# Kernel tuning notes

Measured on AMD Instinct MI355X. Metric: run time of the kernel, lower is better.

## Reference

```python
import jax, jax.numpy as jnp
import numpy as np

B, N, C, H = 4, 2048, 1024, 16
HD = C // H            # head dim = 64
HALF = HD // 2         # complex pairs per head = 32
VR = 32.0              # virtual_resolution
THETA = 10.0           # rope_theta


def _init_freqs():
    # mirrors init_3d_freqs_unified + per-axis replication with small noise
    rng = np.random.default_rng(0)
    idx = np.arange(HALF, dtype=np.float32)
    base = 1.0 / THETA ** (2.0 * idx / HD)                 # [HALF]
    angles = rng.uniform(0, 2 * np.pi, size=(H, 1)).astype(np.float32)
    per_head = base[None, :] * np.cos(angles)              # [H, HALF]
    freqs = np.repeat(per_head[None], 3, axis=0)           # [3, H, HALF]
    freqs = freqs + rng.normal(0, 0.01, freqs.shape).astype(np.float32)
    return jnp.asarray(freqs.reshape(3, H * HALF), dtype=jnp.float32)


def setup_inputs() -> dict:
    key = jax.random.key(0)
    ks = jax.random.split(key, 7)
    x = jax.random.normal(ks[0], (B, N, C), dtype=jnp.float32)
    t_x = jax.random.uniform(ks[1], (N,), dtype=jnp.float32)
    t_y = jax.random.uniform(ks[2], (N,), dtype=jnp.float32)
    t_z = jax.random.uniform(ks[3], (N,), dtype=jnp.float32)
    w_qkv = jax.random.normal(ks[4], (3 * C, C), dtype=jnp.float32) * (C ** -0.5)
    w_proj = jax.random.normal(ks[5], (C, C), dtype=jnp.float32) * (C ** -0.5)
    b_proj = jnp.zeros((C,), dtype=jnp.float32)
    freqs = _init_freqs()
    return {"x": x, "t_x": t_x, "t_y": t_y, "t_z": t_z,
            "w_qkv": w_qkv, "w_proj": w_proj, "b_proj": b_proj, "freqs": freqs}


def _normalize(t):
    # normalize_point_coords_3d with 'virtual_resolution'
    return (t - t.min()) / (t.max() - t.min() + 1e-8) * VR


def reference(x, t_x, t_y, t_z, w_qkv, w_proj, b_proj, freqs):
    # QKV projection (no bias)
    qkv = (x @ w_qkv.T).reshape(B, N, 3, H, HD).transpose(2, 0, 3, 1, 4)  # [3,B,H,N,HD]
    q, k, v = qkv[0], qkv[1], qkv[2]

    # mixed 3D RoPE angles: outer(t_axis, freqs[axis]) summed over axes
    tx, ty, tz = _normalize(t_x), _normalize(t_y), _normalize(t_z)
    ang = (tx[:, None] * freqs[0] + ty[:, None] * freqs[1] + tz[:, None] * freqs[2])  # [N, H*HALF]
    ang = ang.reshape(N, H, HALF).transpose(1, 0, 2)       # [H, N, HALF]
    cos, sin = jnp.cos(ang), jnp.sin(ang)

    def rotate(t):
        # complex multiply (a+ib)*(cos+isin) on even/odd pairs of last dim
        tr = t.reshape(B, H, N, HALF, 2)
        a, b = tr[..., 0], tr[..., 1]
        ra = a * cos - b * sin
        rb = a * sin + b * cos
        return jnp.stack([ra, rb], axis=-1).reshape(B, H, N, HD)

    q = rotate(q)
    k = rotate(k)

    scale = HD ** -0.5
    attn = jax.nn.softmax(jnp.einsum('bhnd,bhmd->bhnm', q * scale, k), axis=-1)
    out = jnp.einsum('bhnm,bhmd->bhnd', attn, v).transpose(0, 2, 1, 3).reshape(B, N, C)
    return out @ w_proj.T + b_proj
```

## Files before the change

kernel.cpp:

```cpp
#include <hip/hip_runtime.h>
#include <math.h>

#define BB 4
#define NN 2048
#define CC 1024
#define HH 16
#define HD 64
#define HALF 32
#define MM (BB*NN)
#define K3 (3*CC)
#define NF (HH*HALF)
#define NT (NN/64)

typedef __attribute__((ext_vector_type(8))) short bf16x8;
typedef __attribute__((ext_vector_type(4))) float f32x4;
typedef __attribute__((ext_vector_type(16))) float f32x16;
typedef __attribute__((ext_vector_type(4))) unsigned short u16x4;
typedef __attribute__((ext_vector_type(8))) unsigned short u16x8;
typedef __attribute__((ext_vector_type(4))) unsigned int u32x4;

#if __has_builtin(__builtin_amdgcn_exp2f)
#define EXP2(x) __builtin_amdgcn_exp2f(x)
#else
#define EXP2(x) exp2f(x)
#endif
#define AS1 __attribute__((address_space(1)))
#define AS3 __attribute__((address_space(3)))

__device__ __forceinline__ unsigned short f2bf(float f) {
    unsigned int u = __float_as_uint(f);
    unsigned int r = (u + 0x7FFFu + ((u >> 16) & 1u)) >> 16;
    return (unsigned short)r;
}

__global__ __launch_bounds__(256) void tnorm_kernel(const float* t_x, const float* t_y,
                                                    const float* t_z, float* tnorm) {
    int a = blockIdx.x;
    const float* t = (a == 0) ? t_x : ((a == 1) ? t_y : t_z);
    __shared__ float smn[256], smx[256];
    float mn = 1e30f, mx = -1e30f;
    for (int i = threadIdx.x; i < NN; i += 256) {
        float v = t[i];
        mn = fminf(mn, v);
        mx = fmaxf(mx, v);
    }
    smn[threadIdx.x] = mn; smx[threadIdx.x] = mx;
    __syncthreads();
    for (int s = 128; s > 0; s >>= 1) {
        if (threadIdx.x < s) {
            smn[threadIdx.x] = fminf(smn[threadIdx.x], smn[threadIdx.x + s]);
            smx[threadIdx.x] = fmaxf(smx[threadIdx.x], smx[threadIdx.x + s]);
        }
        __syncthreads();
    }
    float lo = smn[0];
    float sc = 32.0f / (smx[0] - lo + 1e-8f);
    for (int i = threadIdx.x; i < NN; i += 256)
        tnorm[a * NN + i] = (t[i] - lo) * sc;
}

__global__ __launch_bounds__(512) void angle_kernel(const float* freqs, const float* tnorm,
                                                    float* csT) {
    int n = blockIdx.x;
    int hf = threadIdx.x;
    float ang = tnorm[n] * freqs[hf]
              + tnorm[NN + n] * freqs[NF + hf]
              + tnorm[2 * NN + n] * freqs[2 * NF + hf];
    float2 cs;
    cs.x = cosf(ang);
    cs.y = sinf(ang);
    *(float2*)(csT + 2 * ((size_t)n * NF + hf)) = cs;
}

__global__ __launch_bounds__(256) void cvt_kernel(const float* __restrict__ src,
                                                  unsigned short* __restrict__ dst, int n) {
    int i = (blockIdx.x * 256 + threadIdx.x) * 8;
    if (i < n) {
        float4 a = *(const float4*)(src + i);
        float4 b = *(const float4*)(src + i + 4);
        u16x8 o;
        o[0] = f2bf(a.x); o[1] = f2bf(a.y); o[2] = f2bf(a.z); o[3] = f2bf(a.w);
        o[4] = f2bf(b.x); o[5] = f2bf(b.y); o[6] = f2bf(b.z); o[7] = f2bf(b.w);
        *(u16x8*)(dst + i) = o;
    }
}

__global__ __launch_bounds__(256) void qkv_gemm_kernel(const unsigned short* __restrict__ A,
                                                       const unsigned short* __restrict__ Bw,
                                                       const float* __restrict__ csT,
                                                       unsigned short* __restrict__ qb,
                                                       unsigned short* __restrict__ kb,
                                                       unsigned short* __restrict__ vbT) {
    __shared__ unsigned short Asl[128 * 64];
    __shared__ unsigned short Bsl[128 * 64];
    const int tid = threadIdx.x;
    const int wv = tid >> 6, l = tid & 63;
    const int wm = wv >> 1, wn = wv & 1;
    const int lg = l >> 4, l15 = l & 15;
    const int bid = blockIdx.x;
    const int wgid = (bid & 7) * 192 + (bid >> 3);
    const int m0 = (wgid & 63) * 128;
    const int n0 = (wgid >> 6) * 128;

    f32x4 acc[4][4];
#pragma unroll
    for (int i = 0; i < 4; i++)
#pragma unroll
        for (int j = 0; j < 4; j++) acc[i][j] = f32x4{0.f, 0.f, 0.f, 0.f};

    for (int kt = 0; kt < CC; kt += 64) {
        __syncthreads();
#pragma unroll
        for (int i = 0; i < 4; i++) {
            int c = (wv * 4 + i) * 64 + l;
            int r = c >> 3, kc = c & 7;
            int sc = kt + ((kc ^ (r & 7)) * 8);
            __builtin_amdgcn_global_load_lds(
                (AS1 void*)(A + (size_t)(m0 + r) * CC + sc),
                (AS3 void*)(&Asl[(wv * 4 + i) * 512]), 16, 0, 0);
            __builtin_amdgcn_global_load_lds(
                (AS1 void*)(Bw + (size_t)(n0 + r) * CC + sc),
                (AS3 void*)(&Bsl[(wv * 4 + i) * 512]), 16, 0, 0);
        }
        __syncthreads();
#pragma unroll
        for (int kc = 0; kc < 2; kc++) {
            bf16x8 af[4], bfr[4];
#pragma unroll
            for (int mi = 0; mi < 4; mi++) {
                int r = wm * 64 + mi * 16 + l15;
                af[mi] = *(const bf16x8*)(&Asl[r * 64 + (((kc * 4 + lg) ^ (r & 7)) * 8)]);
            }
#pragma unroll
            for (int nj = 0; nj < 4; nj++) {
                int r = wn * 64 + nj * 16 + l15;
                bfr[nj] = *(const bf16x8*)(&Bsl[r * 64 + (((kc * 4 + lg) ^ (r & 7)) * 8)]);
            }
#pragma unroll
            for (int mi = 0; mi < 4; mi++)
#pragma unroll
                for (int nj = 0; nj < 4; nj++)
                    acc[mi][nj] = __builtin_amdgcn_mfma_f32_16x16x32_bf16(af[mi], bfr[nj], acc[mi][nj], 0, 0, 0);
        }
    }
    const int b_ = m0 >> 11;
    const int nrow0 = (m0 & (NN - 1));
#pragma unroll
    for (int nj = 0; nj < 4; nj++) {
        int oc = n0 + wn * 64 + nj * 16 + l15;
        int s = oc >> 10;
        int rr = oc & 1023;
        int h = rr >> 6;
        int d = rr & 63;
        int f = d >> 1;
#pragma unroll
        for (int mi = 0; mi < 4; mi++) {
            f32x4 v = acc[mi][nj];
            if (s == 2) {
                u16x4 vv;
#pragma unroll
                for (int reg = 0; reg < 4; reg++) vv[reg] = f2bf(v[reg]);
                int nb = nrow0 + wm * 64 + mi * 16 + lg * 4;
                *(u16x4*)(vbT + ((size_t)((b_ * HH + h) * HD + d)) * NN + nb) = vv;
            } else {
#pragma unroll
                for (int reg = 0; reg < 4; reg++) {
                    int m = m0 + wm * 64 + mi * 16 + lg * 4 + reg;
                    int n = m & (NN - 1);
                    float val = v[reg];
                    float partner = __shfl_xor(val, 1);
                    size_t base = (((size_t)(b_ * HH + h)) * NN + n) * HD + d;
                    float2 cs2 = *(const float2*)(csT + 2 * ((size_t)n * NF + h * HALF + f));
                    float res = ((d & 1) == 0) ? (val * cs2.x - partner * cs2.y)
                                               : (val * cs2.x + partner * cs2.y);
                    if (s == 0) res *= 0.18033688011112043f;
                    (s == 0 ? qb : kb)[base] = f2bf(res);
                }
            }
        }
    }
}

template<int BUF>
__device__ __forceinline__ void attn_iter(
    unsigned short* LB, bool do_stage, int wv, int l31,
    const unsigned short*& kn0, const unsigned short*& kn1,
    const unsigned short*& vn0, const unsigned short*& vn1,
    const int (&so)[4], const bf16x8 (&qfA)[4], const bf16x8 (&qfB)[4],
    const f32x16& Z, const bf16x8& ones,
    f32x16& OA0, f32x16& OA1, f32x16& OB0, f32x16& OB1,
    f32x16& SsA, f32x16& SsB) {
    if (do_stage) {
        const int nb = (BUF ^ 1) * 4096;
        __builtin_amdgcn_global_load_lds((AS1 void*)kn0, (AS3 void*)(&LB[nb + (wv * 2 + 0) * 512]), 16, 0, 0);
        __builtin_amdgcn_global_load_lds((AS1 void*)kn1, (AS3 void*)(&LB[nb + (wv * 2 + 1) * 512]), 16, 0, 0);
        __builtin_amdgcn_global_load_lds((AS1 void*)vn0, (AS3 void*)(&LB[8192 + nb + (wv * 2 + 0) * 512]), 16, 0, 0);
        __builtin_amdgcn_global_load_lds((AS1 void*)vn1, (AS3 void*)(&LB[8192 + nb + (wv * 2 + 1) * 512]), 16, 0, 0);
        kn0 += 4096; kn1 += 4096; vn0 += 64; vn1 += 64;
    }
    f32x16 sA0, sA1, sB0, sB1;
    __builtin_amdgcn_s_setprio(1);
    {
        bf16x8 a0 = *(const bf16x8*)(LB + BUF * 4096 + l31 * 64 + so[0]);
        bf16x8 a1 = *(const bf16x8*)(LB + BUF * 4096 + (32 + l31) * 64 + so[0]);
        sA0 = __builtin_amdgcn_mfma_f32_32x32x16_bf16(a0, qfA[0], Z, 0, 0, 0);
        sA1 = __builtin_amdgcn_mfma_f32_32x32x16_bf16(a1, qfA[0], Z, 0, 0, 0);
        sB0 = __builtin_amdgcn_mfma_f32_32x32x16_bf16(a0, qfB[0], Z, 0, 0, 0);
        sB1 = __builtin_amdgcn_mfma_f32_32x32x16_bf16(a1, qfB[0], Z, 0, 0, 0);
    }
#pragma unroll
    for (int dc = 1; dc < 4; dc++) {
        bf16x8 a0 = *(const bf16x8*)(LB + BUF * 4096 + l31 * 64 + so[dc]);
        bf16x8 a1 = *(const bf16x8*)(LB + BUF * 4096 + (32 + l31) * 64 + so[dc]);
        sA0 = __builtin_amdgcn_mfma_f32_32x32x16_bf16(a0, qfA[dc], sA0, 0, 0, 0);
        sA1 = __builtin_amdgcn_mfma_f32_32x32x16_bf16(a1, qfA[dc], sA1, 0, 0, 0);
        sB0 = __builtin_amdgcn_mfma_f32_32x32x16_bf16(a0, qfB[dc], sB0, 0, 0, 0);
        sB1 = __builtin_amdgcn_mfma_f32_32x32x16_bf16(a1, qfB[dc], sB1, 0, 0, 0);
    }
    __builtin_amdgcn_s_setprio(0);
#pragma unroll
    for (int r = 0; r < 16; r++) {
        sA0[r] = EXP2(sA0[r]); sA1[r] = EXP2(sA1[r]);
        sB0[r] = EXP2(sB0[r]); sB1[r] = EXP2(sB1[r]);
    }
#pragma unroll
    for (int r = 0; r < 8; r++) {
        unsigned u0, u1, u2, u3;
        asm("v_cvt_pk_bf16_f32 %0, %1, %2" : "=v"(u0) : "v"(sA0[2 * r]), "v"(sA0[2 * r + 1]));
        asm("v_cvt_pk_bf16_f32 %0, %1, %2" : "=v"(u1) : "v"(sA1[2 * r]), "v"(sA1[2 * r + 1]));
        asm("v_cvt_pk_bf16_f32 %0, %1, %2" : "=v"(u2) : "v"(sB0[2 * r]), "v"(sB0[2 * r + 1]));
        asm("v_cvt_pk_bf16_f32 %0, %1, %2" : "=v"(u3) : "v"(sB1[2 * r]), "v"(sB1[2 * r + 1]));
        sA0[2 * r] = __uint_as_float(u0);
        sA1[2 * r] = __uint_as_float(u1);
        sB0[2 * r] = __uint_as_float(u2);
        sB1[2 * r] = __uint_as_float(u3);
    }
    __builtin_amdgcn_s_setprio(1);
#pragma unroll
    for (int kc = 0; kc < 4; kc++) {
        const int bs = (kc & 1) * 8;
        bf16x8 pfA, pfB;
        {
            float e0 = (kc < 2) ? sA0[bs + 0] : sA1[bs + 0];
            float e4 = (kc < 2) ? sA0[bs + 4] : sA1[bs + 4];
            float e2 = (kc < 2) ? sA0[bs + 2] : sA1[bs + 2];
            float e6 = (kc < 2) ? sA0[bs + 6] : sA1[bs + 6];
            auto uA = __builtin_amdgcn_permlane32_swap(__float_as_uint(e0), __float_as_uint(e4), false, false);
            auto uB = __builtin_amdgcn_permlane32_swap(__float_as_uint(e2), __float_as_uint(e6), false, false);
            u32x4 t; t.x = uA[0]; t.y = uB[0]; t.z = uA[1]; t.w = uB[1];
            pfA = __builtin_bit_cast(bf16x8, t);
        }
        {
            float e0 = (kc < 2) ? sB0[bs + 0] : sB1[bs + 0];
            float e4 = (kc < 2) ? sB0[bs + 4] : sB1[bs + 4];
            float e2 = (kc < 2) ? sB0[bs + 2] : sB1[bs + 2];
            float e6 = (kc < 2) ? sB0[bs + 6] : sB1[bs + 6];
            auto uA = __builtin_amdgcn_permlane32_swap(__float_as_uint(e0), __float_as_uint(e4), false, false);
            auto uB = __builtin_amdgcn_permlane32_swap(__float_as_uint(e2), __float_as_uint(e6), false, false);
            u32x4 t; t.x = uA[0]; t.y = uB[0]; t.z = uA[1]; t.w = uB[1];
            pfB = __builtin_bit_cast(bf16x8, t);
        }
        bf16x8 va  = *(const bf16x8*)(LB + 8192 + BUF * 4096 + l31 * 64 + so[kc]);
        bf16x8 vb2 = *(const bf16x8*)(LB + 8192 + BUF * 4096 + (32 + l31) * 64 + so[kc]);
        OA0 = __builtin_amdgcn_mfma_f32_32x32x16_bf16(va,  pfA, OA0, 0, 0, 0);
        OA1 = __builtin_amdgcn_mfma_f32_32x32x16_bf16(vb2, pfA, OA1, 0, 0, 0);
        OB0 = __builtin_amdgcn_mfma_f32_32x32x16_bf16(va,  pfB, OB0, 0, 0, 0);
        OB1 = __builtin_amdgcn_mfma_f32_32x32x16_bf16(vb2, pfB, OB1, 0, 0, 0);
        SsA = __builtin_amdgcn_mfma_f32_32x32x16_bf16(ones, pfA, SsA, 0, 0, 0);
        SsB = __builtin_amdgcn_mfma_f32_32x32x16_bf16(ones, pfB, SsB, 0, 0, 0);
    }
    __builtin_amdgcn_s_setprio(0);
    __syncthreads();
}

__global__ __launch_bounds__(256, 2) void attn_mfma_kernel(const unsigned short* __restrict__ qbp,
                                                           const unsigned short* __restrict__ kbp,
                                                           const unsigned short* __restrict__ vtp,
                                                           unsigned short* __restrict__ aout) {
    __shared__ unsigned short LB[4 * 4096];
    const int tid = threadIdx.x;
    const int wv = tid >> 6;
    const int l = tid & 63;
    const int l31 = l & 31, hi = l >> 5;

    const int wg = blockIdx.x;
    const int Lidx = (wg & 7) * 64 + (wg >> 3);
    const int bh = Lidx >> 3;
    const int q0 = (Lidx & 7) * 256;

    const unsigned short* qp = qbp + (size_t)bh * (NN * HD);
    const unsigned short* kp = kbp + (size_t)bh * (NN * HD);
    const unsigned short* vp = vtp + (size_t)bh * (NN * HD);

    const int r0 = (wv * 2 + 0) * 8 + (l >> 3);
    const int r1 = (wv * 2 + 1) * 8 + (l >> 3);
    const int c0 = ((l & 7) ^ (r0 & 7)) * 8;
    const int c1 = ((l & 7) ^ (r1 & 7)) * 8;
    const unsigned short* kn0 = kp + r0 * HD + c0;
    const unsigned short* kn1 = kp + r1 * HD + c1;
    const unsigned short* vn0 = vp + (size_t)r0 * NN + c0;
    const unsigned short* vn1 = vp + (size_t)r1 * NN + c1;

    __builtin_amdgcn_global_load_lds((AS1 void*)kn0, (AS3 void*)(&LB[(wv * 2 + 0) * 512]), 16, 0, 0);
    __builtin_amdgcn_global_load_lds((AS1 void*)kn1, (AS3 void*)(&LB[(wv * 2 + 1) * 512]), 16, 0, 0);
    __builtin_amdgcn_global_load_lds((AS1 void*)vn0, (AS3 void*)(&LB[8192 + (wv * 2 + 0) * 512]), 16, 0, 0);
    __builtin_amdgcn_global_load_lds((AS1 void*)vn1, (AS3 void*)(&LB[8192 + (wv * 2 + 1) * 512]), 16, 0, 0);
    kn0 += 4096; kn1 += 4096; vn0 += 64; vn1 += 64;

    const unsigned short* qr = qp + (size_t)(q0 + wv * 64 + l31) * HD;
    bf16x8 qfA[4], qfB[4];
#pragma unroll
    for (int dc = 0; dc < 4; dc++) {
        qfA[dc] = *(const bf16x8*)(qr + dc * 16 + hi * 8);
        qfB[dc] = *(const bf16x8*)(qr + 32 * HD + dc * 16 + hi * 8);
    }

    int so[4];
#pragma unroll
    for (int i = 0; i < 4; i++) so[i] = ((2 * i + hi) ^ (l31 & 7)) * 8;

    f32x16 Z;
#pragma unroll
    for (int r = 0; r < 16; r++) Z[r] = 0.0f;
    f32x16 OA0 = Z, OA1 = Z, OB0 = Z, OB1 = Z, SsA = Z, SsB = Z;
    bf16x8 ones;
#pragma unroll
    for (int j = 0; j < 8; j++) ones[j] = (short)0x3F80;

    __syncthreads();

    for (int ktb = 0; ktb < NT; ktb += 2) {
        attn_iter<0>(LB, true, wv, l31, kn0, kn1, vn0, vn1, so, qfA, qfB,
                     Z, ones, OA0, OA1, OB0, OB1, SsA, SsB);
        attn_iter<1>(LB, ktb + 2 < NT, wv, l31, kn0, kn1, vn0, vn1, so, qfA, qfB,
                     Z, ones, OA0, OA1, OB0, OB1, SsA, SsB);
    }

    const int b_ = bh >> 4, hh = bh & 15;
    const float invA = 1.0f / SsA[0], invB = 1.0f / SsB[0];
    const size_t mrowA = (size_t)(b_ * NN + q0 + wv * 64 + l31) * CC + hh * HD;
    const size_t mrowB = mrowA + (size_t)32 * CC;
#pragma unroll
    for (int rq = 0; rq < 4; rq++) {
        u16x4 a0, a1, b0, b1;
#pragma unroll
        for (int j = 0; j < 4; j++) {
            a0[j] = f2bf(OA0[rq * 4 + j] * invA);
            a1[j] = f2bf(OA1[rq * 4 + j] * invA);
            b0[j] = f2bf(OB0[rq * 4 + j] * invB);
            b1[j] = f2bf(OB1[rq * 4 + j] * invB);
        }
        *(u16x4*)(aout + mrowA + rq * 8 + hi * 4) = a0;
        *(u16x4*)(aout + mrowA + 32 + rq * 8 + hi * 4) = a1;
        *(u16x4*)(aout + mrowB + rq * 8 + hi * 4) = b0;
        *(u16x4*)(aout + mrowB + 32 + rq * 8 + hi * 4) = b1;
    }
}

__global__ __launch_bounds__(256) void proj_gemm_kernel(const unsigned short* __restrict__ A,
                                                        const unsigned short* __restrict__ Bw,
                                                        const float* __restrict__ bp,
                                                        float* __restrict__ out) {
    __shared__ unsigned short Asl[128 * 64];
    __shared__ unsigned short Bsl[128 * 64];
    const int tid = threadIdx.x;
    const int wv = tid >> 6, l = tid & 63;
    const int wm = wv >> 1, wn = wv & 1;
    const int lg = l >> 4, l15 = l & 15;
    const int bid = blockIdx.x;
    const int wgid = (bid & 7) * 64 + (bid >> 3);
    const int m0 = (wgid & 63) * 128;
    const int n0 = (wgid >> 6) * 128;

    f32x4 acc[4][4];
#pragma unroll
    for (int i = 0; i < 4; i++)
#pragma unroll
        for (int j = 0; j < 4; j++) acc[i][j] = f32x4{0.f, 0.f, 0.f, 0.f};

    for (int kt = 0; kt < CC; kt += 64) {
        __syncthreads();
#pragma unroll
        for (int i = 0; i < 4; i++) {
            int c = (wv * 4 + i) * 64 + l;
            int r = c >> 3, kc = c & 7;
            int sc = kt + ((kc ^ (r & 7)) * 8);
            __builtin_amdgcn_global_load_lds(
                (AS1 void*)(A + (size_t)(m0 + r) * CC + sc),
                (AS3 void*)(&Asl[(wv * 4 + i) * 512]), 16, 0, 0);
            __builtin_amdgcn_global_load_lds(
                (AS1 void*)(Bw + (size_t)(n0 + r) * CC + sc),
                (AS3 void*)(&Bsl[(wv * 4 + i) * 512]), 16, 0, 0);
        }
        __syncthreads();
#pragma unroll
        for (int kc = 0; kc < 2; kc++) {
            bf16x8 af[4], bfr[4];
#pragma unroll
            for (int mi = 0; mi < 4; mi++) {
                int r = wm * 64 + mi * 16 + l15;
                af[mi] = *(const bf16x8*)(&Asl[r * 64 + (((kc * 4 + lg) ^ (r & 7)) * 8)]);
            }
#pragma unroll
            for (int nj = 0; nj < 4; nj++) {
                int r = wn * 64 + nj * 16 + l15;
                bfr[nj] = *(const bf16x8*)(&Bsl[r * 64 + (((kc * 4 + lg) ^ (r & 7)) * 8)]);
            }
#pragma unroll
            for (int mi = 0; mi < 4; mi++)
#pragma unroll
                for (int nj = 0; nj < 4; nj++)
                    acc[mi][nj] = __builtin_amdgcn_mfma_f32_16x16x32_bf16(af[mi], bfr[nj], acc[mi][nj], 0, 0, 0);
        }
    }
    float bias[4];
#pragma unroll
    for (int nj = 0; nj < 4; nj++) bias[nj] = bp[n0 + wn * 64 + nj * 16 + l15];
#pragma unroll
    for (int mi = 0; mi < 4; mi++)
#pragma unroll
        for (int nj = 0; nj < 4; nj++) {
            int oc = n0 + wn * 64 + nj * 16 + l15;
#pragma unroll
            for (int reg = 0; reg < 4; reg++) {
                int m = m0 + wm * 64 + mi * 16 + lg * 4 + reg;
                out[(size_t)m * CC + oc] = acc[mi][nj][reg] + bias[nj];
            }
        }
}

extern "C" void kernel_launch(void* const* d_in, const int* in_sizes, int n_in,
                              void* d_out, int out_size, void* d_ws, size_t ws_size,
                              hipStream_t stream) {
    const float* x      = (const float*)d_in[0];
    const float* t_x    = (const float*)d_in[1];
    const float* t_y    = (const float*)d_in[2];
    const float* t_z    = (const float*)d_in[3];
    const float* w_qkv  = (const float*)d_in[4];
    const float* w_proj = (const float*)d_in[5];
    const float* b_proj = (const float*)d_in[6];
    const float* freqs  = (const float*)d_in[7];
    float* out = (float*)d_out;

    unsigned short* xb     = (unsigned short*)d_ws;
    unsigned short* wqkvb  = xb + (size_t)MM * CC;
    unsigned short* wprojb = wqkvb + (size_t)K3 * CC;
    unsigned short* qbuf   = wprojb + (size_t)CC * CC;
    unsigned short* kbuf   = qbuf + (size_t)BB * HH * NN * HD;
    unsigned short* vbT    = kbuf + (size_t)BB * HH * NN * HD;
    unsigned short* attnb  = vbT + (size_t)BB * HH * NN * HD;
    float* csT   = (float*)(attnb + (size_t)MM * CC);
    float* tnorm = csT + (size_t)2 * NN * NF;

    tnorm_kernel<<<3, 256, 0, stream>>>(t_x, t_y, t_z, tnorm);
    angle_kernel<<<NN, 512, 0, stream>>>(freqs, tnorm, csT);
    cvt_kernel<<<(MM * CC) / 2048, 256, 0, stream>>>(x, xb, MM * CC);
    cvt_kernel<<<(K3 * CC) / 2048, 256, 0, stream>>>(w_qkv, wqkvb, K3 * CC);
    cvt_kernel<<<(CC * CC) / 2048, 256, 0, stream>>>(w_proj, wprojb, CC * CC);
    qkv_gemm_kernel<<<1536, 256, 0, stream>>>(xb, wqkvb, csT, qbuf, kbuf, vbT);
    attn_mfma_kernel<<<512, 256, 0, stream>>>(qbuf, kbuf, vbT, attnb);
    proj_gemm_kernel<<<512, 256, 0, stream>>>(attnb, wprojb, b_proj, out);
}
```

Before: 230.6 us.

## Halve attention query tile per wave and drop XCD swizzle in GEMMs

The attention kernel now gives each wave 32 query rows instead of 64, so each block covers 128 queries. This doubles the grid to 1024 blocks and raises launch bounds to 4 blocks per SIMD to improve occupancy and latency hiding, at the cost of loading each K/V tile twice as often. The QKV and projection GEMMs replace the XCD-aware block index swizzle with a plain 2D grid. That may change L2 locality across chiplets.

```diff
diff --git a/kernel.cpp b/kernel.cpp
--- a/kernel.cpp
+++ b/kernel.cpp
@@ -97,10 +97,7 @@
     const int wv = tid >> 6, l = tid & 63;
     const int wm = wv >> 1, wn = wv & 1;
     const int lg = l >> 4, l15 = l & 15;
-    const int bid = blockIdx.x;
-    const int wgid = (bid & 7) * 192 + (bid >> 3);
-    const int m0 = (wgid & 63) * 128;
-    const int n0 = (wgid >> 6) * 128;
+    const int m0 = blockIdx.x * 128, n0 = blockIdx.y * 128;
 
     f32x4 acc[4][4];
 #pragma unroll
@@ -186,10 +183,9 @@
     unsigned short* LB, bool do_stage, int wv, int l31,
     const unsigned short*& kn0, const unsigned short*& kn1,
     const unsigned short*& vn0, const unsigned short*& vn1,
-    const int (&so)[4], const bf16x8 (&qfA)[4], const bf16x8 (&qfB)[4],
+    const int (&so)[4], const bf16x8 (&qf)[4],
     const f32x16& Z, const bf16x8& ones,
-    f32x16& OA0, f32x16& OA1, f32x16& OB0, f32x16& OB1,
-    f32x16& SsA, f32x16& SsB) {
+    f32x16& O0, f32x16& O1, f32x16& Ss) {
     if (do_stage) {
         const int nb = (BUF ^ 1) * 4096;
         __builtin_amdgcn_global_load_lds((AS1 void*)kn0, (AS3 void*)(&LB[nb + (wv * 2 + 0) * 512]), 16, 0, 0);
@@ -198,82 +194,58 @@
         __builtin_amdgcn_global_load_lds((AS1 void*)vn1, (AS3 void*)(&LB[8192 + nb + (wv * 2 + 1) * 512]), 16, 0, 0);
         kn0 += 4096; kn1 += 4096; vn0 += 64; vn1 += 64;
     }
-    f32x16 sA0, sA1, sB0, sB1;
+    f32x16 s0, s1;
     __builtin_amdgcn_s_setprio(1);
     {
         bf16x8 a0 = *(const bf16x8*)(LB + BUF * 4096 + l31 * 64 + so[0]);
         bf16x8 a1 = *(const bf16x8*)(LB + BUF * 4096 + (32 + l31) * 64 + so[0]);
-        sA0 = __builtin_amdgcn_mfma_f32_32x32x16_bf16(a0, qfA[0], Z, 0, 0, 0);
-        sA1 = __builtin_amdgcn_mfma_f32_32x32x16_bf16(a1, qfA[0], Z, 0, 0, 0);
-        sB0 = __builtin_amdgcn_mfma_f32_32x32x16_bf16(a0, qfB[0], Z, 0, 0, 0);
-        sB1 = __builtin_amdgcn_mfma_f32_32x32x16_bf16(a1, qfB[0], Z, 0, 0, 0);
+        s0 = __builtin_amdgcn_mfma_f32_32x32x16_bf16(a0, qf[0], Z, 0, 0, 0);
+        s1 = __builtin_amdgcn_mfma_f32_32x32x16_bf16(a1, qf[0], Z, 0, 0, 0);
     }
 #pragma unroll
     for (int dc = 1; dc < 4; dc++) {
         bf16x8 a0 = *(const bf16x8*)(LB + BUF * 4096 + l31 * 64 + so[dc]);
         bf16x8 a1 = *(const bf16x8*)(LB + BUF * 4096 + (32 + l31) * 64 + so[dc]);
-        sA0 = __builtin_amdgcn_mfma_f32_32x32x16_bf16(a0, qfA[dc], sA0, 0, 0, 0);
-        sA1 = __builtin_amdgcn_mfma_f32_32x32x16_bf16(a1, qfA[dc], sA1, 0, 0, 0);
-        sB0 = __builtin_amdgcn_mfma_f32_32x32x16_bf16(a0, qfB[dc], sB0, 0, 0, 0);
-        sB1 = __builtin_amdgcn_mfma_f32_32x32x16_bf16(a1, qfB[dc], sB1, 0, 0, 0);
+        s0 = __builtin_amdgcn_mfma_f32_32x32x16_bf16(a0, qf[dc], s0, 0, 0, 0);
+        s1 = __builtin_amdgcn_mfma_f32_32x32x16_bf16(a1, qf[dc], s1, 0, 0, 0);
     }
     __builtin_amdgcn_s_setprio(0);
 #pragma unroll
-    for (int r = 0; r < 16; r++) {
-        sA0[r] = EXP2(sA0[r]); sA1[r] = EXP2(sA1[r]);
-        sB0[r] = EXP2(sB0[r]); sB1[r] = EXP2(sB1[r]);
-    }
+    for (int r = 0; r < 16; r++) { s0[r] = EXP2(s0[r]); s1[r] = EXP2(s1[r]); }
 #pragma unroll
     for (int r = 0; r < 8; r++) {
-        unsigned u0, u1, u2, u3;
-        asm("v_cvt_pk_bf16_f32 %0, %1, %2" : "=v"(u0) : "v"(sA0[2 * r]), "v"(sA0[2 * r + 1]));
-        asm("v_cvt_pk_bf16_f32 %0, %1, %2" : "=v"(u1) : "v"(sA1[2 * r]), "v"(sA1[2 * r + 1]));
-        asm("v_cvt_pk_bf16_f32 %0, %1, %2" : "=v"(u2) : "v"(sB0[2 * r]), "v"(sB0[2 * r + 1]));
-        asm("v_cvt_pk_bf16_f32 %0, %1, %2" : "=v"(u3) : "v"(sB1[2 * r]), "v"(sB1[2 * r + 1]));
-        sA0[2 * r] = __uint_as_float(u0);
-        sA1[2 * r] = __uint_as_float(u1);
-        sB0[2 * r] = __uint_as_float(u2);
-        sB1[2 * r] = __uint_as_float(u3);
+        unsigned u0, u1;
+        asm("v_cvt_pk_bf16_f32 %0, %1, %2" : "=v"(u0) : "v"(s0[2 * r]), "v"(s0[2 * r + 1]));
+        asm("v_cvt_pk_bf16_f32 %0, %1, %2" : "=v"(u1) : "v"(s1[2 * r]), "v"(s1[2 * r + 1]));
+        s0[2 * r] = __uint_as_float(u0);
+        s1[2 * r] = __uint_as_float(u1);
     }
     __builtin_amdgcn_s_setprio(1);
 #pragma unroll
     for (int kc = 0; kc < 4; kc++) {
         const int bs = (kc & 1) * 8;
-        bf16x8 pfA, pfB;
+        bf16x8 pf;
         {
-            float e0 = (kc < 2) ? sA0[bs + 0] : sA1[bs + 0];
-            float e4 = (kc < 2) ? sA0[bs + 4] : sA1[bs + 4];
-            float e2 = (kc < 2) ? sA0[bs + 2] : sA1[bs + 2];
-            float e6 = (kc < 2) ? sA0[bs + 6] : sA1[bs + 6];
+            float e0 = (kc < 2) ? s0[bs + 0] : s1[bs + 0];
+            float e4 = (kc < 2) ? s0[bs + 4] : s1[bs + 4];
+            float e2 = (kc < 2) ? s0[bs + 2] : s1[bs + 2];
+            float e6 = (kc < 2) ? s0[bs + 6] : s1[bs + 6];
             auto uA = __builtin_amdgcn_permlane32_swap(__float_as_uint(e0), __float_as_uint(e4), false, false);
             auto uB = __builtin_amdgcn_permlane32_swap(__float_as_uint(e2), __float_as_uint(e6), false, false);
             u32x4 t; t.x = uA[0]; t.y = uB[0]; t.z = uA[1]; t.w = uB[1];
-            pfA = __builtin_bit_cast(bf16x8, t);
-        }
-        {
-            float e0 = (kc < 2) ? sB0[bs + 0] : sB1[bs + 0];
-            float e4 = (kc < 2) ? sB0[bs + 4] : sB1[bs + 4];
-            float e2 = (kc < 2) ? sB0[bs + 2] : sB1[bs + 2];
-            float e6 = (kc < 2) ? sB0[bs + 6] : sB1[bs + 6];
-            auto uA = __builtin_amdgcn_permlane32_swap(__float_as_uint(e0), __float_as_uint(e4), false, false);
-            auto uB = __builtin_amdgcn_permlane32_swap(__float_as_uint(e2), __float_as_uint(e6), false, false);
-            u32x4 t; t.x = uA[0]; t.y = uB[0]; t.z = uA[1]; t.w = uB[1];
-            pfB = __builtin_bit_cast(bf16x8, t);
+            pf = __builtin_bit_cast(bf16x8, t);
         }
         bf16x8 va  = *(const bf16x8*)(LB + 8192 + BUF * 4096 + l31 * 64 + so[kc]);
         bf16x8 vb2 = *(const bf16x8*)(LB + 8192 + BUF * 4096 + (32 + l31) * 64 + so[kc]);
-        OA0 = __builtin_amdgcn_mfma_f32_32x32x16_bf16(va,  pfA, OA0, 0, 0, 0);
-        OA1 = __builtin_amdgcn_mfma_f32_32x32x16_bf16(vb2, pfA, OA1, 0, 0, 0);
-        OB0 = __builtin_amdgcn_mfma_f32_32x32x16_bf16(va,  pfB, OB0, 0, 0, 0);
-        OB1 = __builtin_amdgcn_mfma_f32_32x32x16_bf16(vb2, pfB, OB1, 0, 0, 0);
-        SsA = __builtin_amdgcn_mfma_f32_32x32x16_bf16(ones, pfA, SsA, 0, 0, 0);
-        SsB = __builtin_amdgcn_mfma_f32_32x32x16_bf16(ones, pfB, SsB, 0, 0, 0);
+        O0 = __builtin_amdgcn_mfma_f32_32x32x16_bf16(va,  pf, O0, 0, 0, 0);
+        O1 = __builtin_amdgcn_mfma_f32_32x32x16_bf16(vb2, pf, O1, 0, 0, 0);
+        Ss = __builtin_amdgcn_mfma_f32_32x32x16_bf16(ones, pf, Ss, 0, 0, 0);
     }
     __builtin_amdgcn_s_setprio(0);
     __syncthreads();
 }
 
-__global__ __launch_bounds__(256, 2) void attn_mfma_kernel(const unsigned short* __restrict__ qbp,
+__global__ __launch_bounds__(256, 4) void attn_mfma_kernel(const unsigned short* __restrict__ qbp,
                                                            const unsigned short* __restrict__ kbp,
                                                            const unsigned short* __restrict__ vtp,
                                                            unsigned short* __restrict__ aout) {
@@ -284,9 +256,9 @@
     const int l31 = l & 31, hi = l >> 5;
 
     const int wg = blockIdx.x;
-    const int Lidx = (wg & 7) * 64 + (wg >> 3);
-    const int bh = Lidx >> 3;
-    const int q0 = (Lidx & 7) * 256;
+    const int Lidx = (wg & 7) * 128 + (wg >> 3);
+    const int bh = Lidx >> 4;
+    const int q0 = (Lidx & 15) * 128;
 
     const unsigned short* qp = qbp + (size_t)bh * (NN * HD);
     const unsigned short* kp = kbp + (size_t)bh * (NN * HD);
@@ -307,13 +279,11 @@
     __builtin_amdgcn_global_load_lds((AS1 void*)vn1, (AS3 void*)(&LB[8192 + (wv * 2 + 1) * 512]), 16, 0, 0);
     kn0 += 4096; kn1 += 4096; vn0 += 64; vn1 += 64;
 
-    const unsigned short* qr = qp + (size_t)(q0 + wv * 64 + l31) * HD;
-    bf16x8 qfA[4], qfB[4];
-#pragma unroll
-    for (int dc = 0; dc < 4; dc++) {
-        qfA[dc] = *(const bf16x8*)(qr + dc * 16 + hi * 8);
-        qfB[dc] = *(const bf16x8*)(qr + 32 * HD + dc * 16 + hi * 8);
-    }
+    const unsigned short* qr = qp + (size_t)(q0 + wv * 32 + l31) * HD;
+    bf16x8 qf[4];
+#pragma unroll
+    for (int dc = 0; dc < 4; dc++)
+        qf[dc] = *(const bf16x8*)(qr + dc * 16 + hi * 8);
 
     int so[4];
 #pragma unroll
@@ -322,7 +292,7 @@
     f32x16 Z;
 #pragma unroll
     for (int r = 0; r < 16; r++) Z[r] = 0.0f;
-    f32x16 OA0 = Z, OA1 = Z, OB0 = Z, OB1 = Z, SsA = Z, SsB = Z;
+    f32x16 O0 = Z, O1 = Z, Ss = Z;
     bf16x8 ones;
 #pragma unroll
     for (int j = 0; j < 8; j++) ones[j] = (short)0x3F80;
@@ -330,30 +300,25 @@
     __syncthreads();
 
     for (int ktb = 0; ktb < NT; ktb += 2) {
-        attn_iter<0>(LB, true, wv, l31, kn0, kn1, vn0, vn1, so, qfA, qfB,
-                     Z, ones, OA0, OA1, OB0, OB1, SsA, SsB);
-        attn_iter<1>(LB, ktb + 2 < NT, wv, l31, kn0, kn1, vn0, vn1, so, qfA, qfB,
-                     Z, ones, OA0, OA1, OB0, OB1, SsA, SsB);
+        attn_iter<0>(LB, true, wv, l31, kn0, kn1, vn0, vn1, so, qf,
+                     Z, ones, O0, O1, Ss);
+        attn_iter<1>(LB, ktb + 2 < NT, wv, l31, kn0, kn1, vn0, vn1, so, qf,
+                     Z, ones, O0, O1, Ss);
     }
 
     const int b_ = bh >> 4, hh = bh & 15;
-    const float invA = 1.0f / SsA[0], invB = 1.0f / SsB[0];
-    const size_t mrowA = (size_t)(b_ * NN + q0 + wv * 64 + l31) * CC + hh * HD;
-    const size_t mrowB = mrowA + (size_t)32 * CC;
+    const float inv = 1.0f / Ss[0];
+    const size_t mrow = (size_t)(b_ * NN + q0 + wv * 32 + l31) * CC + hh * HD;
 #pragma unroll
     for (int rq = 0; rq < 4; rq++) {
-        u16x4 a0, a1, b0, b1;
+        u16x4 o0, o1;
 #pragma unroll
         for (int j = 0; j < 4; j++) {
-            a0[j] = f2bf(OA0[rq * 4 + j] * invA);
-            a1[j] = f2bf(OA1[rq * 4 + j] * invA);
-            b0[j] = f2bf(OB0[rq * 4 + j] * invB);
-            b1[j] = f2bf(OB1[rq * 4 + j] * invB);
-        }
-        *(u16x4*)(aout + mrowA + rq * 8 + hi * 4) = a0;
-        *(u16x4*)(aout + mrowA + 32 + rq * 8 + hi * 4) = a1;
-        *(u16x4*)(aout + mrowB + rq * 8 + hi * 4) = b0;
-        *(u16x4*)(aout + mrowB + 32 + rq * 8 + hi * 4) = b1;
+            o0[j] = f2bf(O0[rq * 4 + j] * inv);
+            o1[j] = f2bf(O1[rq * 4 + j] * inv);
+        }
+        *(u16x4*)(aout + mrow + rq * 8 + hi * 4) = o0;
+        *(u16x4*)(aout + mrow + 32 + rq * 8 + hi * 4) = o1;
     }
 }
 
@@ -367,10 +332,7 @@
     const int wv = tid >> 6, l = tid & 63;
     const int wm = wv >> 1, wn = wv & 1;
     const int lg = l >> 4, l15 = l & 15;
-    const int bid = blockIdx.x;
-    const int wgid = (bid & 7) * 64 + (bid >> 3);
-    const int m0 = (wgid & 63) * 128;
-    const int n0 = (wgid >> 6) * 128;
+    const int m0 = blockIdx.x * 128, n0 = blockIdx.y * 128;
 
     f32x4 acc[4][4];
 #pragma unroll
@@ -457,7 +419,8 @@
     cvt_kernel<<<(MM * CC) / 2048, 256, 0, stream>>>(x, xb, MM * CC);
     cvt_kernel<<<(K3 * CC) / 2048, 256, 0, stream>>>(w_qkv, wqkvb, K3 * CC);
     cvt_kernel<<<(CC * CC) / 2048, 256, 0, stream>>>(w_proj, wprojb, CC * CC);
-    qkv_gemm_kernel<<<1536, 256, 0, stream>>>(xb, wqkvb, csT, qbuf, kbuf, vbT);
-    attn_mfma_kernel<<<512, 256, 0, stream>>>(qbuf, kbuf, vbT, attnb);
-    proj_gemm_kernel<<<512, 256, 0, stream>>>(attnb, wprojb, b_proj, out);
-}
+    qkv_gemm_kernel<<<dim3(MM / 128, K3 / 128), 256, 0, stream>>>(xb, wqkvb, csT,
+                                                                  qbuf, kbuf, vbT);
+    attn_mfma_kernel<<<1024, 256, 0, stream>>>(qbuf, kbuf, vbT, attnb);
+    proj_gemm_kernel<<<dim3(MM / 128, CC / 128), 256, 0, stream>>>(attnb, wprojb, b_proj, out);
+}
```

New measurement: 222.7 us. 1.04x faster.
